# Optimization experiments

Hardware: AMD Instinct MI355X
Metric: run time of the kernel (lower is better)

## Reference

```python
import jax, jax.numpy as jnp
import numpy as np


def _gcn_conv(h, src, dst, W, b, n):
    # PyG GCNConv: x @ W, then symmetric-normalized aggregation with self-loops
    deg = jax.ops.segment_sum(jnp.ones(src.shape[0], h.dtype), dst, num_segments=n)
    dinv = jax.lax.rsqrt(jnp.maximum(deg, 1.0))  # deg >= 1 because self-loops are included
    norm = dinv[src] * dinv[dst]                 # [E]
    m = (h @ W)[src] * norm[:, None]             # gather + scale
    return jax.ops.segment_sum(m, dst, num_segments=n) + b


def setup_inputs() -> dict:
    key = jax.random.key(0)
    N, E, F, H, L, V = 50000, 800000, 128, 256, 64, 128
    ks = jax.random.split(key, 16)
    s = lambda fan_in: 1.0 / np.sqrt(fan_in)
    return {
        "x": jax.random.randint(ks[0], (N,), 0, V),
        "edge_index": jax.random.randint(ks[1], (2, E), 0, N),
        "eps": jax.random.normal(ks[2], (N, L), jnp.float32),
        "emb": jax.random.normal(ks[3], (V, F), jnp.float32),
        "W1": jax.random.normal(ks[4], (F, H), jnp.float32) * s(F),
        "b1": jnp.zeros((H,), jnp.float32),
        "W2": jax.random.normal(ks[5], (H, H), jnp.float32) * s(H),
        "b2": jnp.zeros((H,), jnp.float32),
        "Wmu": jax.random.normal(ks[6], (H, L), jnp.float32) * s(H),
        "bmu": jnp.zeros((L,), jnp.float32),
        "Wlv": jax.random.normal(ks[7], (H, L), jnp.float32) * s(H),
        "blv": jnp.zeros((L,), jnp.float32),
        "W3": jax.random.normal(ks[8], (L, H), jnp.float32) * s(L),
        "b3": jnp.zeros((H,), jnp.float32),
        "W4": jax.random.normal(ks[9], (H, V), jnp.float32) * s(H),
        "b4": jnp.zeros((V,), jnp.float32),
        "Wcap": jax.random.normal(ks[10], (L, 1), jnp.float32) * s(L),
        "bcap": jnp.zeros((1,), jnp.float32),
    }


def reference(x, edge_index, eps, emb, W1, b1, W2, b2, Wmu, bmu, Wlv, blv, W3, b3, W4, b4, Wcap, bcap):
    n = x.shape[0]
    loops = jnp.arange(n, dtype=edge_index.dtype)
    src = jnp.concatenate([edge_index[0], loops])  # add self-loops once, reuse
    dst = jnp.concatenate([edge_index[1], loops])

    h = emb[x]                                      # [N, F] embedding lookup
    h = jax.nn.relu(_gcn_conv(h, src, dst, W1, b1, n))
    h = jax.nn.relu(_gcn_conv(h, src, dst, W2, b2, n))
    mu = h @ Wmu + bmu
    logvar = h @ Wlv + blv
    z = mu + eps * jnp.exp(0.5 * logvar)            # reparameterize
    recon_x = jax.nn.relu(z @ W3 + b3) @ W4 + b4    # decode
    capitalize = jax.nn.sigmoid(z @ Wcap + bcap)
    return recon_x, capitalize, mu, logvar
```

## Files before the change

### kernel.cpp

```cpp
#include <hip/hip_runtime.h>
#include <math.h>


typedef __attribute__((ext_vector_type(8))) short bf16x8;
typedef __attribute__((ext_vector_type(8))) unsigned short u16x8;
typedef __attribute__((ext_vector_type(4))) float f32x4;

__device__ inline unsigned short f2bf(float x) {
    unsigned u = __float_as_uint(x);
    return (unsigned short)((u + 0x7FFFu + ((u >> 16) & 1u)) >> 16);
}
__device__ inline float bf2f(unsigned short h) {
    return __uint_as_float(((unsigned)h) << 16);
}

__global__ __launch_bounds__(256) void k_deg_count(const int* __restrict__ dst,
                                                   int* __restrict__ degint, int E) {
    int e = blockIdx.x * 256 + threadIdx.x;
    if (e < E) atomicAdd(&degint[dst[e]], 1);
}

#define SCAN_BLOCK 1024
__global__ __launch_bounds__(SCAN_BLOCK) void k_scan_local(
        const int* __restrict__ degint, int* __restrict__ row_ptr,
        int* __restrict__ bsum, float* __restrict__ dinv, int N) {
    __shared__ int s[SCAN_BLOCK];
    int gid = blockIdx.x * SCAN_BLOCK + threadIdx.x;
    int d = (gid < N) ? (degint[gid] + 1) : 0;
    if (gid < N) dinv[gid] = rsqrtf((float)d);
    s[threadIdx.x] = d;
    __syncthreads();
    for (int off = 1; off < SCAN_BLOCK; off <<= 1) {
        int t = (threadIdx.x >= off) ? s[threadIdx.x - off] : 0;
        __syncthreads();
        s[threadIdx.x] += t;
        __syncthreads();
    }
    if (gid < N) row_ptr[gid] = s[threadIdx.x] - d;
    if (threadIdx.x == SCAN_BLOCK - 1) bsum[blockIdx.x] = s[SCAN_BLOCK - 1];
}

__global__ void k_scan_bsum(int* __restrict__ bsum, int nb) {
    if (blockIdx.x == 0 && threadIdx.x == 0) {
        int acc = 0;
        for (int i = 0; i < nb; ++i) { int v = bsum[i]; bsum[i] = acc; acc += v; }
    }
}

__global__ __launch_bounds__(256) void k_scan_add(int* __restrict__ row_ptr,
                                                  const int* __restrict__ bsum,
                                                  int N, int T) {
    int gid = blockIdx.x * 256 + threadIdx.x;
    if (gid < N) row_ptr[gid] += bsum[gid / SCAN_BLOCK];
    if (gid == 0) row_ptr[N] = T;
}

__global__ __launch_bounds__(256) void k_fill(
        const int* __restrict__ src, const int* __restrict__ dst,
        const int* __restrict__ x, const float* __restrict__ dinv,
        const int* __restrict__ row_ptr, int* __restrict__ cursor,
        int4* __restrict__ pack, int E, int N) {
    const int base = (blockIdx.x * 256 + threadIdx.x) * 4;
#pragma unroll
    for (int j = 0; j < 4; ++j) {
        int e = base + j;
        if (e < E) {
            int s = src[e], d = dst[e];
            float w = dinv[s] * dinv[d];
            int pos = row_ptr[d] + atomicAdd(&cursor[d], 1);
            pack[pos] = make_int4(__float_as_int(w), s, x[s], 0);
        } else if (e < E + N) {
            int i = e - E;
            float di = dinv[i];
            int pos = row_ptr[i] + atomicAdd(&cursor[i], 1);
            pack[pos] = make_int4(__float_as_int(di * di), i, x[i], 0);
        }
    }
}

__global__ __launch_bounds__(256) void k_cvt_all(
        const float* __restrict__ B0, unsigned short* __restrict__ h0, int K0, int N0,
        const float* __restrict__ B1, unsigned short* __restrict__ h1, int K1, int N1,
        const float* __restrict__ B2, unsigned short* __restrict__ h2, int K2, int N2,
        const float* __restrict__ B3, unsigned short* __restrict__ h3, int K3, int N3,
        const float* __restrict__ B4, unsigned short* __restrict__ h4, int K4, int N4) {
    const float* B; unsigned short* Bh; int K, Ncol;
    switch (blockIdx.y) {
        case 0: B = B0; Bh = h0; K = K0; Ncol = N0; break;
        case 1: B = B1; Bh = h1; K = K1; Ncol = N1; break;
        case 2: B = B2; Bh = h2; K = K2; Ncol = N2; break;
        case 3: B = B3; Bh = h3; K = K3; Ncol = N3; break;
        default: B = B4; Bh = h4; K = K4; Ncol = N4; break;
    }
    int i = blockIdx.x * 256 + threadIdx.x;
    if (i >= K * Ncol) return;
    int k = i / Ncol, n = i - k * Ncol;
    Bh[(long)n * K + k] = f2bf(B[i]);
}

__global__ __launch_bounds__(256) void k_gemm_f32t(
        const float* __restrict__ A, const float* __restrict__ B,
        unsigned short* __restrict__ CbT, int M, int K, int Ncol) {
    constexpr int BM = 64, BN = 64, BK = 16;
    __shared__ float As[BK][BM];
    __shared__ float Bs[BK][BN];
    const int tid = threadIdx.x;
    const int tx = tid & 15, ty = tid >> 4;
    const int rowBase = blockIdx.x * BM;
    const int colBase = blockIdx.y * BN;
    const int lr = tid >> 2, lc4 = tid & 3;
    const int br = tid >> 4, bc4 = tid & 15;
    const int arow = rowBase + lr;
    const int K4 = K >> 2, N4 = Ncol >> 2;
    const float4* A4 = (const float4*)A;
    const float4* B4 = (const float4*)B;
    float acc[4][4] = {{0.f}};
    for (int k0 = 0; k0 < K; k0 += BK) {
        float4 av = make_float4(0.f, 0.f, 0.f, 0.f);
        if (arow < M) av = A4[(long)arow * K4 + (k0 >> 2) + lc4];
        As[lc4 * 4 + 0][lr] = av.x;
        As[lc4 * 4 + 1][lr] = av.y;
        As[lc4 * 4 + 2][lr] = av.z;
        As[lc4 * 4 + 3][lr] = av.w;
        float4 bv = B4[(long)(k0 + br) * N4 + (colBase >> 2) + bc4];
        *(float4*)&Bs[br][bc4 * 4] = bv;
        __syncthreads();
#pragma unroll
        for (int k = 0; k < BK; ++k) {
            float4 a4v = *(const float4*)&As[k][ty * 4];
            float4 b4v = *(const float4*)&Bs[k][tx * 4];
            float aa[4] = {a4v.x, a4v.y, a4v.z, a4v.w};
            float bb[4] = {b4v.x, b4v.y, b4v.z, b4v.w};
#pragma unroll
            for (int i = 0; i < 4; ++i)
#pragma unroll
                for (int j = 0; j < 4; ++j)
                    acc[i][j] = fmaf(aa[i], bb[j], acc[i][j]);
        }
        __syncthreads();
    }
#pragma unroll
    for (int i = 0; i < 4; ++i) {
        int row = rowBase + ty * 4 + i;
        if (row < M) {
#pragma unroll
            for (int c = 0; c < 4; ++c) {
                int col = colBase + tx * 4 + c;
                CbT[(long)col * M + row] = f2bf(acc[i][c]);
            }
        }
    }
}

__global__ __launch_bounds__(256) void k_coef(
        const int4* __restrict__ pack, const int* __restrict__ row_ptr,
        unsigned short* __restrict__ cb, int N) {
    const int wave = threadIdx.x >> 6;
    const int lane = threadIdx.x & 63;
    const int node = blockIdx.x * 4 + wave;
    if (node >= N) return;
    const int tok0 = lane, tok1 = lane + 64;
    float c0 = 0.f, c1 = 0.f;
    const int beg = row_ptr[node], end = row_ptr[node + 1];
    int e = beg;
    for (; e + 4 <= end; e += 4) {
        int4 p0 = pack[e];
        int4 p1 = pack[e + 1];
        int4 p2 = pack[e + 2];
        int4 p3 = pack[e + 3];
        c0 += (p0.z == tok0) ? __int_as_float(p0.x) : 0.f;
        c1 += (p0.z == tok1) ? __int_as_float(p0.x) : 0.f;
        c0 += (p1.z == tok0) ? __int_as_float(p1.x) : 0.f;
        c1 += (p1.z == tok1) ? __int_as_float(p1.x) : 0.f;
        c0 += (p2.z == tok0) ? __int_as_float(p2.x) : 0.f;
        c1 += (p2.z == tok1) ? __int_as_float(p2.x) : 0.f;
        c0 += (p3.z == tok0) ? __int_as_float(p3.x) : 0.f;
        c1 += (p3.z == tok1) ? __int_as_float(p3.x) : 0.f;
    }
    for (; e < end; ++e) {
        int4 p = pack[e];
        c0 += (p.z == tok0) ? __int_as_float(p.x) : 0.f;
        c1 += (p.z == tok1) ? __int_as_float(p.x) : 0.f;
    }
    const long base = (long)node * 128;
    cb[base + lane]      = f2bf(c0);
    cb[base + lane + 64] = f2bf(c1);
}

template<bool RELU>
__global__ __launch_bounds__(256) void k_gemm_bn128(
        const unsigned short* __restrict__ A, const unsigned short* __restrict__ Bt,
        const float* __restrict__ bias, unsigned short* __restrict__ Cb,
        int M, int K, int Ncol) {
    __shared__ unsigned short Ash[64][40];
    __shared__ unsigned short Bsh[128][40];
    const int tid = threadIdx.x;
    const int lane = tid & 63, w = tid >> 6;
    const int fr = lane & 15, quad = lane >> 4;
    const int wm0 = w * 16;
    const int rowBase = blockIdx.x * 64;
    const int colBase = blockIdx.y * 128;

    const int arow = tid >> 2;
    const int aseg = (tid & 3) << 3;
    int agrow = rowBase + arow; if (agrow >= M) agrow = M - 1;
    const long abase = (long)agrow * K + aseg;
    const int brow = tid >> 1;
    const int bseg = (tid & 1) << 4;
    const long bbase = (long)(colBase + brow) * K + bseg;

    f32x4 acc[8];
#pragma unroll
    for (int j = 0; j < 8; ++j) acc[j] = (f32x4){0.f, 0.f, 0.f, 0.f};

    for (int k0 = 0; k0 < K; k0 += 32) {
        *(bf16x8*)&Ash[arow][aseg]     = *(const bf16x8*)&A[abase + k0];
        *(bf16x8*)&Bsh[brow][bseg]     = *(const bf16x8*)&Bt[bbase + k0];
        *(bf16x8*)&Bsh[brow][bseg + 8] = *(const bf16x8*)&Bt[bbase + k0 + 8];
        __syncthreads();
        bf16x8 af = *(const bf16x8*)&Ash[wm0 + fr][quad * 8];
#pragma unroll
        for (int j = 0; j < 8; ++j) {
            bf16x8 bhf = *(const bf16x8*)&Bsh[j * 16 + fr][quad * 8];
            acc[j] = __builtin_amdgcn_mfma_f32_16x16x32_bf16(af, bhf, acc[j], 0, 0, 0);
        }
        __syncthreads();
    }

#pragma unroll
    for (int j = 0; j < 8; ++j) {
        const int col = colBase + j * 16 + fr;
        const float bv = bias[col];
#pragma unroll
        for (int r = 0; r < 4; ++r) {
            const int row = rowBase + wm0 + quad * 4 + r;
            if (row < M) {
                float v = acc[j][r] + bv;
                if (RELU) v = fmaxf(v, 0.f);
                Cb[(long)row * Ncol + col] = f2bf(v);
            }
        }
    }
}

__global__ __launch_bounds__(256) void k_gemm_heads(
        const unsigned short* __restrict__ A, const unsigned short* __restrict__ Bt,
        const float* __restrict__ bmu, const float* __restrict__ blv,
        const float* __restrict__ eps, const float* __restrict__ Wcap,
        const float* __restrict__ bcap, float* __restrict__ mu,
        float* __restrict__ lv, unsigned short* __restrict__ Zh,
        float* __restrict__ cap, int M) {
    constexpr int K = 256;
    __shared__ unsigned short Ash[64][40];
    __shared__ unsigned short Bsh[128][40];
    const int tid = threadIdx.x;
    const int lane = tid & 63, w = tid >> 6;
    const int fr = lane & 15, quad = lane >> 4;
    const int wm0 = w * 16;
    const int rowBase = blockIdx.x * 64;

    const int arow = tid >> 2;
    const int aseg = (tid & 3) << 3;
    int agrow = rowBase + arow; if (agrow >= M) agrow = M - 1;
    const long abase = (long)agrow * K + aseg;
    const int brow = tid >> 1;
    const int bseg = (tid & 1) << 4;
    const long bbase = (long)brow * K + bseg;

    f32x4 acc[8];
#pragma unroll
    for (int j = 0; j < 8; ++j) acc[j] = (f32x4){0.f, 0.f, 0.f, 0.f};

    for (int k0 = 0; k0 < K; k0 += 32) {
        *(bf16x8*)&Ash[arow][aseg] = *(const bf16x8*)&A[abase + k0];
        *(bf16x8*)&Bsh[brow][bseg]     = *(const bf16x8*)&Bt[bbase + k0];
        *(bf16x8*)&Bsh[brow][bseg + 8] = *(const bf16x8*)&Bt[bbase + k0 + 8];
        __syncthreads();
        bf16x8 ahf = *(const bf16x8*)&Ash[wm0 + fr][quad * 8];
#pragma unroll
        for (int j = 0; j < 8; ++j) {
            bf16x8 bhf = *(const bf16x8*)&Bsh[j * 16 + fr][quad * 8];
            acc[j] = __builtin_amdgcn_mfma_f32_16x16x32_bf16(ahf, bhf, acc[j], 0, 0, 0);
        }
        __syncthreads();
    }

    float capacc[4] = {0.f, 0.f, 0.f, 0.f};
#pragma unroll
    for (int j = 0; j < 4; ++j) {
        const int c = j * 16 + fr;
        const float bm = bmu[c], bl = blv[c];
        const float wc = Wcap[c];
#pragma unroll
        for (int r = 0; r < 4; ++r) {
            const int row = rowBase + wm0 + quad * 4 + r;
            if (row < M) {
                const long o = (long)row * 64 + c;
                float mv = acc[j][r] + bm;
                float lvv = acc[j + 4][r] + bl;
                mu[o] = mv;
                lv[o] = lvv;
                float zz = fmaf(eps[o], expf(0.5f * lvv), mv);
                Zh[o] = f2bf(zz);
                capacc[r] = fmaf(zz, wc, capacc[r]);
            }
        }
    }
    const float b0 = bcap[0];
#pragma unroll
    for (int r = 0; r < 4; ++r) {
        float v = capacc[r];
        v += __shfl_xor(v, 1, 64);
        v += __shfl_xor(v, 2, 64);
        v += __shfl_xor(v, 4, 64);
        v += __shfl_xor(v, 8, 64);
        if (fr == 0) {
            const int row = rowBase + wm0 + quad * 4 + r;
            if (row < M) cap[row] = 1.f / (1.f + expf(-(v + b0)));
        }
    }
}

__global__ __launch_bounds__(256) void k_gemm_decode(
        const unsigned short* __restrict__ Zh, const unsigned short* __restrict__ W3t,
        const unsigned short* __restrict__ W4t, const float* __restrict__ b3,
        const float* __restrict__ b4, float* __restrict__ recon, int M) {
    __shared__ unsigned short Zs[64][40];
    __shared__ unsigned short Bsh[256][40];
    __shared__ unsigned short Ts[64][264];
    const int tid = threadIdx.x;
    const int lane = tid & 63, w = tid >> 6;
    const int fr = lane & 15, quad = lane >> 4;
    const int wm0 = w * 16;
    const int rowBase = blockIdx.x * 64;

    const int zrow = tid & 63;
    const int zseg = (tid >> 6) << 3;
    int zgrow = rowBase + zrow; if (zgrow >= M) zgrow = M - 1;

    f32x4 acc1[16];
#pragma unroll
    for (int j = 0; j < 16; ++j) acc1[j] = (f32x4){0.f, 0.f, 0.f, 0.f};
    for (int k0 = 0; k0 < 64; k0 += 32) {
        *(bf16x8*)&Zs[zrow][zseg] = *(const bf16x8*)&Zh[(long)zgrow * 64 + k0 + zseg];
        {
            const long wb = (long)tid * 64 + k0;
            *(bf16x8*)&Bsh[tid][0]  = *(const bf16x8*)&W3t[wb];
            *(bf16x8*)&Bsh[tid][8]  = *(const bf16x8*)&W3t[wb + 8];
            *(bf16x8*)&Bsh[tid][16] = *(const bf16x8*)&W3t[wb + 16];
            *(bf16x8*)&Bsh[tid][24] = *(const bf16x8*)&W3t[wb + 24];
        }
        __syncthreads();
        bf16x8 af = *(const bf16x8*)&Zs[wm0 + fr][quad * 8];
#pragma unroll
        for (int j = 0; j < 16; ++j) {
            bf16x8 bf = *(const bf16x8*)&Bsh[j * 16 + fr][quad * 8];
            acc1[j] = __builtin_amdgcn_mfma_f32_16x16x32_bf16(af, bf, acc1[j], 0, 0, 0);
        }
        __syncthreads();
    }

#pragma unroll
    for (int j = 0; j < 16; ++j) {
        const int col = j * 16 + fr;
        const float bv = b3[col];
#pragma unroll
        for (int r = 0; r < 4; ++r) {
            const int rl = wm0 + quad * 4 + r;
            Ts[rl][col] = f2bf(fmaxf(acc1[j][r] + bv, 0.f));
        }
    }
    __syncthreads();

    f32x4 acc2[8];
#pragma unroll
    for (int j = 0; j < 8; ++j) acc2[j] = (f32x4){0.f, 0.f, 0.f, 0.f};
    const int br2 = tid >> 1;
    const int bs2 = (tid & 1) << 4;
    for (int k0 = 0; k0 < 256; k0 += 32) {
        const long wb = (long)br2 * 256 + k0 + bs2;
        *(bf16x8*)&Bsh[br2][bs2]     = *(const bf16x8*)&W4t[wb];
        *(bf16x8*)&Bsh[br2][bs2 + 8] = *(const bf16x8*)&W4t[wb + 8];
        __syncthreads();
        bf16x8 at = *(const bf16x8*)&Ts[wm0 + fr][k0 + quad * 8];
#pragma unroll
        for (int j = 0; j < 8; ++j) {
            bf16x8 bf = *(const bf16x8*)&Bsh[j * 16 + fr][quad * 8];
            acc2[j] = __builtin_amdgcn_mfma_f32_16x16x32_bf16(at, bf, acc2[j], 0, 0, 0);
        }
        __syncthreads();
    }

#pragma unroll
    for (int j = 0; j < 8; ++j) {
        const int col = j * 16 + fr;
        const float bv = b4[col];
#pragma unroll
        for (int r = 0; r < 4; ++r) {
            const int row = rowBase + wm0 + quad * 4 + r;
            if (row < M) recon[(long)row * 128 + col] = acc2[j][r] + bv;
        }
    }
}

__global__ __launch_bounds__(256) void k_agg_nb(
        const unsigned short* __restrict__ h1, const int* __restrict__ row_ptr,
        const int2* __restrict__ pk2, unsigned short* __restrict__ Ob, int N) {
    const int wave = threadIdx.x >> 6;
    const int lane = threadIdx.x & 63;
    const int node = blockIdx.x * 4 + wave;
    if (node >= N) return;
    const int half = lane >> 5;
    const int col  = lane & 31;
    const u16x8* hrow = (const u16x8*)h1;
    float acc[8] = {0.f, 0.f, 0.f, 0.f, 0.f, 0.f, 0.f, 0.f};
    const int beg = row_ptr[node], end = row_ptr[node + 1];
    int e = beg;
    for (; e + 8 <= end; e += 8) {
        int2 q0 = pk2[2 * (e + 0 + half)];
        int2 q1 = pk2[2 * (e + 2 + half)];
        int2 q2 = pk2[2 * (e + 4 + half)];
        int2 q3 = pk2[2 * (e + 6 + half)];
        u16x8 v0 = hrow[(long)q0.y * 32 + col];
        u16x8 v1 = hrow[(long)q1.y * 32 + col];
        u16x8 v2 = hrow[(long)q2.y * 32 + col];
        u16x8 v3 = hrow[(long)q3.y * 32 + col];
        float w0 = __int_as_float(q0.x), w1 = __int_as_float(q1.x);
        float w2 = __int_as_float(q2.x), w3 = __int_as_float(q3.x);
#pragma unroll
        for (int c = 0; c < 8; ++c) {
            acc[c] = fmaf(bf2f(v0[c]), w0, acc[c]);
            acc[c] = fmaf(bf2f(v1[c]), w1, acc[c]);
            acc[c] = fmaf(bf2f(v2[c]), w2, acc[c]);
            acc[c] = fmaf(bf2f(v3[c]), w3, acc[c]);
        }
    }
    for (; e + 2 <= end; e += 2) {
        int2 q = pk2[2 * (e + half)];
        float w = __int_as_float(q.x);
        u16x8 v = hrow[(long)q.y * 32 + col];
#pragma unroll
        for (int c = 0; c < 8; ++c) acc[c] = fmaf(bf2f(v[c]), w, acc[c]);
    }
    if (e < end) {
        int2 q = pk2[2 * e];
        float w = (half == 0) ? __int_as_float(q.x) : 0.f;
        u16x8 v = hrow[(long)q.y * 32 + col];
#pragma unroll
        for (int c = 0; c < 8; ++c) acc[c] = fmaf(bf2f(v[c]), w, acc[c]);
    }
#pragma unroll
    for (int c = 0; c < 8; ++c) acc[c] += __shfl_xor(acc[c], 32, 64);
    if (lane < 32) {
        u16x8 o;
#pragma unroll
        for (int c = 0; c < 8; ++c) o[c] = f2bf(acc[c]);
        ((u16x8*)Ob)[(long)node * 32 + col] = o;
    }
}

extern "C" void kernel_launch(void* const* d_in, const int* in_sizes, int n_in,
                              void* d_out, int out_size, void* d_ws, size_t ws_size,
                              hipStream_t stream) {
    const int*   x    = (const int*)d_in[0];
    const int*   ei   = (const int*)d_in[1];
    const float* eps  = (const float*)d_in[2];
    const float* emb  = (const float*)d_in[3];
    const float* W1   = (const float*)d_in[4];
    const float* b1   = (const float*)d_in[5];
    const float* W2   = (const float*)d_in[6];
    const float* b2   = (const float*)d_in[7];
    const float* Wmu  = (const float*)d_in[8];
    const float* bmu  = (const float*)d_in[9];
    const float* Wlv  = (const float*)d_in[10];
    const float* blv  = (const float*)d_in[11];
    const float* W3   = (const float*)d_in[12];
    const float* b3   = (const float*)d_in[13];
    const float* W4   = (const float*)d_in[14];
    const float* b4   = (const float*)d_in[15];
    const float* Wcap = (const float*)d_in[16];
    const float* bcap = (const float*)d_in[17];

    const int N = in_sizes[0];
    const int E = in_sizes[1] / 2;
    const int H = in_sizes[5];
    const int L = in_sizes[9];
    const int V = in_sizes[15];
    const int F = in_sizes[4] / H;
    const int T = E + N;

    const int* src = ei;
    const int* dst = ei + E;

    char* w = (char*)d_ws;
    unsigned short* h1b  = (unsigned short*)w; w += (size_t)N * H * 2;
    unsigned short* a2b  = (unsigned short*)w; w += (size_t)N * H * 2;
    unsigned short* h2b  = (unsigned short*)w; w += (size_t)N * H * 2;
    unsigned short* zh   = (unsigned short*)w; w += (size_t)N * L * 2;
    unsigned short* cb   = (unsigned short*)w; w += (size_t)N * V * 2;
    int*   degint = (int*)w;   w += (size_t)N * 4;
    int*   cursor = (int*)w;   w += (size_t)N * 4;
    int*   rowp   = (int*)w;   w += (size_t)(N + 1) * 4;
    float* dinv   = (float*)w; w += (size_t)N * 4;
    int*   bsum   = (int*)w;   w += 256 * 4;
    int4*  pack   = (int4*)w;  w += (size_t)T * 16;
    unsigned short* tabT = (unsigned short*)w; w += (size_t)H * V * 2;
    unsigned short* W2t  = (unsigned short*)w; w += (size_t)H * H * 2;
    unsigned short* Wml  = (unsigned short*)w; w += (size_t)H * 2 * L * 2;
    unsigned short* W3t  = (unsigned short*)w; w += (size_t)L * H * 2;
    unsigned short* W4t  = (unsigned short*)w; w += (size_t)H * V * 2;

    float* outp    = (float*)d_out;
    float* recon   = outp;
    float* cap     = outp + (size_t)N * V;
    float* mu      = outp + (size_t)N * V + N;
    float* logvar  = mu + (size_t)N * L;

    const int nN  = (N + 255) / 256;
    const int nE  = (E + 255) / 256;
    const int nT4 = (T + 1023) / 1024;
    const int nSc = (N + SCAN_BLOCK - 1) / SCAN_BLOCK;
    const int gM64  = (N + 63) / 64;

    hipMemsetAsync(degint, 0, (size_t)N * 8, stream);
    k_deg_count<<<nE, 256, 0, stream>>>(dst, degint, E);
    k_scan_local<<<nSc, SCAN_BLOCK, 0, stream>>>(degint, rowp, bsum, dinv, N);
    k_scan_bsum<<<1, 64, 0, stream>>>(bsum, nSc);
    k_scan_add<<<nN, 256, 0, stream>>>(rowp, bsum, N, T);
    k_fill<<<nT4, 256, 0, stream>>>(src, dst, x, dinv, rowp, cursor, pack, E, N);

    k_cvt_all<<<dim3((H * H + 255) / 256, 5), 256, 0, stream>>>(
        W2, W2t, H, H,
        Wmu, Wml, H, L,
        Wlv, Wml + (size_t)L * H, H, L,
        W3, W3t, L, H,
        W4, W4t, H, V);

    k_gemm_f32t<<<dim3(V / 64, H / 64), 256, 0, stream>>>(emb, W1, tabT, V, F, H);
    k_coef<<<(N + 3) / 4, 256, 0, stream>>>(pack, rowp, cb, N);
    k_gemm_bn128<true><<<dim3(gM64, H / 128), 256, 0, stream>>>(
        cb, tabT, b1, h1b, N, V, H);

    k_agg_nb<<<(N + 3) / 4, 256, 0, stream>>>(h1b, rowp, (const int2*)pack, a2b, N);
    k_gemm_bn128<true><<<dim3(gM64, H / 128), 256, 0, stream>>>(
        a2b, W2t, b2, h2b, N, H, H);

    k_gemm_heads<<<gM64, 256, 0, stream>>>(
        h2b, Wml, bmu, blv, eps, Wcap, bcap, mu, logvar, zh, cap, N);

    k_gemm_decode<<<gM64, 256, 0, stream>>>(zh, W3t, W4t, b3, b4, recon, N);
}
```

Measured before the change: 399.4 us.

## Fuse heads and decode GEMMs into one kernel and fold block-sum scan

Merges the mu/logvar heads GEMM and the decode MLP into one kernel, so z stays in shared memory instead of being written to and re-read from a global bf16 buffer. The serial single-thread block-sum scan kernel is removed; each scan_add wave now reduces the preceding block sums with shuffles. This saves a kernel launch and a round trip of z through global memory. In exchange the fused kernel uses more shared memory per block, which may lower occupancy, and the in-wave scan only handles up to 64 scan blocks (N up to 65536).

```diff
diff --git a/kernel.cpp b/kernel.cpp
--- a/kernel.cpp
+++ b/kernel.cpp
@@ -40,18 +40,20 @@
     if (threadIdx.x == SCAN_BLOCK - 1) bsum[blockIdx.x] = s[SCAN_BLOCK - 1];
 }
 
-__global__ void k_scan_bsum(int* __restrict__ bsum, int nb) {
-    if (blockIdx.x == 0 && threadIdx.x == 0) {
-        int acc = 0;
-        for (int i = 0; i < nb; ++i) { int v = bsum[i]; bsum[i] = acc; acc += v; }
-    }
-}
-
 __global__ __launch_bounds__(256) void k_scan_add(int* __restrict__ row_ptr,
                                                   const int* __restrict__ bsum,
                                                   int N, int T) {
-    int gid = blockIdx.x * 256 + threadIdx.x;
-    if (gid < N) row_ptr[gid] += bsum[gid / SCAN_BLOCK];
+    const int gid = blockIdx.x * 256 + threadIdx.x;
+    const int myb = (blockIdx.x * 256) / SCAN_BLOCK;
+    const int lane = threadIdx.x & 63;
+    int v = (lane < myb) ? bsum[lane] : 0;
+    v += __shfl_xor(v, 1, 64);
+    v += __shfl_xor(v, 2, 64);
+    v += __shfl_xor(v, 4, 64);
+    v += __shfl_xor(v, 8, 64);
+    v += __shfl_xor(v, 16, 64);
+    v += __shfl_xor(v, 32, 64);
+    if (gid < N) row_ptr[gid] += v;
     if (gid == 0) row_ptr[N] = T;
 }
 
@@ -243,21 +245,31 @@
     }
 }
 
-__global__ __launch_bounds__(256) void k_gemm_heads(
-        const unsigned short* __restrict__ A, const unsigned short* __restrict__ Bt,
+__global__ __launch_bounds__(256) void k_gemm_tail(
+        const unsigned short* __restrict__ A, const unsigned short* __restrict__ Wml,
+        const unsigned short* __restrict__ W3t, const unsigned short* __restrict__ W4t,
         const float* __restrict__ bmu, const float* __restrict__ blv,
         const float* __restrict__ eps, const float* __restrict__ Wcap,
-        const float* __restrict__ bcap, float* __restrict__ mu,
-        float* __restrict__ lv, unsigned short* __restrict__ Zh,
+        const float* __restrict__ bcap, const float* __restrict__ b3,
+        const float* __restrict__ b4, float* __restrict__ mu,
+        float* __restrict__ lv, float* __restrict__ recon,
         float* __restrict__ cap, int M) {
     constexpr int K = 256;
     __shared__ unsigned short Ash[64][40];
-    __shared__ unsigned short Bsh[128][40];
+    __shared__ unsigned short Bsh[256][40];
+    __shared__ unsigned short Zs[64][72];
+    __shared__ unsigned short Ts[64][264];
     const int tid = threadIdx.x;
     const int lane = tid & 63, w = tid >> 6;
     const int fr = lane & 15, quad = lane >> 4;
     const int wm0 = w * 16;
     const int rowBase = blockIdx.x * 64;
+
+    {
+        const int zr = tid >> 2, zc = (tid & 3) * 18;
+#pragma unroll
+        for (int c = 0; c < 18; ++c) Zs[zr][zc + c] = 0;
+    }
 
     const int arow = tid >> 2;
     const int aseg = (tid & 3) << 3;
@@ -272,9 +284,9 @@
     for (int j = 0; j < 8; ++j) acc[j] = (f32x4){0.f, 0.f, 0.f, 0.f};
 
     for (int k0 = 0; k0 < K; k0 += 32) {
-        *(bf16x8*)&Ash[arow][aseg] = *(const bf16x8*)&A[abase + k0];
-        *(bf16x8*)&Bsh[brow][bseg]     = *(const bf16x8*)&Bt[bbase + k0];
-        *(bf16x8*)&Bsh[brow][bseg + 8] = *(const bf16x8*)&Bt[bbase + k0 + 8];
+        *(bf16x8*)&Ash[arow][aseg]     = *(const bf16x8*)&A[abase + k0];
+        *(bf16x8*)&Bsh[brow][bseg]     = *(const bf16x8*)&Wml[bbase + k0];
+        *(bf16x8*)&Bsh[brow][bseg + 8] = *(const bf16x8*)&Wml[bbase + k0 + 8];
         __syncthreads();
         bf16x8 ahf = *(const bf16x8*)&Ash[wm0 + fr][quad * 8];
 #pragma unroll
@@ -293,7 +305,8 @@
         const float wc = Wcap[c];
 #pragma unroll
         for (int r = 0; r < 4; ++r) {
-            const int row = rowBase + wm0 + quad * 4 + r;
+            const int rl = wm0 + quad * 4 + r;
+            const int row = rowBase + rl;
             if (row < M) {
                 const long o = (long)row * 64 + c;
                 float mv = acc[j][r] + bm;
@@ -301,7 +314,7 @@
                 mu[o] = mv;
                 lv[o] = lvv;
                 float zz = fmaf(eps[o], expf(0.5f * lvv), mv);
-                Zh[o] = f2bf(zz);
+                Zs[rl][c] = f2bf(zz);
                 capacc[r] = fmaf(zz, wc, capacc[r]);
             }
         }
@@ -319,30 +332,11 @@
             if (row < M) cap[row] = 1.f / (1.f + expf(-(v + b0)));
         }
     }
-}
-
-__global__ __launch_bounds__(256) void k_gemm_decode(
-        const unsigned short* __restrict__ Zh, const unsigned short* __restrict__ W3t,
-        const unsigned short* __restrict__ W4t, const float* __restrict__ b3,
-        const float* __restrict__ b4, float* __restrict__ recon, int M) {
-    __shared__ unsigned short Zs[64][40];
-    __shared__ unsigned short Bsh[256][40];
-    __shared__ unsigned short Ts[64][264];
-    const int tid = threadIdx.x;
-    const int lane = tid & 63, w = tid >> 6;
-    const int fr = lane & 15, quad = lane >> 4;
-    const int wm0 = w * 16;
-    const int rowBase = blockIdx.x * 64;
-
-    const int zrow = tid & 63;
-    const int zseg = (tid >> 6) << 3;
-    int zgrow = rowBase + zrow; if (zgrow >= M) zgrow = M - 1;
 
     f32x4 acc1[16];
 #pragma unroll
     for (int j = 0; j < 16; ++j) acc1[j] = (f32x4){0.f, 0.f, 0.f, 0.f};
     for (int k0 = 0; k0 < 64; k0 += 32) {
-        *(bf16x8*)&Zs[zrow][zseg] = *(const bf16x8*)&Zh[(long)zgrow * 64 + k0 + zseg];
         {
             const long wb = (long)tid * 64 + k0;
             *(bf16x8*)&Bsh[tid][0]  = *(const bf16x8*)&W3t[wb];
@@ -351,7 +345,7 @@
             *(bf16x8*)&Bsh[tid][24] = *(const bf16x8*)&W3t[wb + 24];
         }
         __syncthreads();
-        bf16x8 af = *(const bf16x8*)&Zs[wm0 + fr][quad * 8];
+        bf16x8 af = *(const bf16x8*)&Zs[wm0 + fr][k0 + quad * 8];
 #pragma unroll
         for (int j = 0; j < 16; ++j) {
             bf16x8 bf = *(const bf16x8*)&Bsh[j * 16 + fr][quad * 8];
@@ -496,7 +490,6 @@
     unsigned short* h1b  = (unsigned short*)w; w += (size_t)N * H * 2;
     unsigned short* a2b  = (unsigned short*)w; w += (size_t)N * H * 2;
     unsigned short* h2b  = (unsigned short*)w; w += (size_t)N * H * 2;
-    unsigned short* zh   = (unsigned short*)w; w += (size_t)N * L * 2;
     unsigned short* cb   = (unsigned short*)w; w += (size_t)N * V * 2;
     int*   degint = (int*)w;   w += (size_t)N * 4;
     int*   cursor = (int*)w;   w += (size_t)N * 4;
@@ -525,7 +518,6 @@
     hipMemsetAsync(degint, 0, (size_t)N * 8, stream);
     k_deg_count<<<nE, 256, 0, stream>>>(dst, degint, E);
     k_scan_local<<<nSc, SCAN_BLOCK, 0, stream>>>(degint, rowp, bsum, dinv, N);
-    k_scan_bsum<<<1, 64, 0, stream>>>(bsum, nSc);
     k_scan_add<<<nN, 256, 0, stream>>>(rowp, bsum, N, T);
     k_fill<<<nT4, 256, 0, stream>>>(src, dst, x, dinv, rowp, cursor, pack, E, N);
 
@@ -545,8 +537,7 @@
     k_gemm_bn128<true><<<dim3(gM64, H / 128), 256, 0, stream>>>(
         a2b, W2t, b2, h2b, N, H, H);
 
-    k_gemm_heads<<<gM64, 256, 0, stream>>>(
-        h2b, Wml, bmu, blv, eps, Wcap, bcap, mu, logvar, zh, cap, N);
-
-    k_gemm_decode<<<gM64, 256, 0, stream>>>(zh, W3t, W4t, b3, b4, recon, N);
-}
+    k_gemm_tail<<<gM64, 256, 0, stream>>>(
+        h2b, Wml, W3t, W4t, bmu, blv, eps, Wcap, bcap, b3, b4,
+        mu, logvar, recon, cap, N);
+}
```

New measurement: 387.2 us. -3.1%, faster.
